# Optimization experiments

Hardware: AMD Instinct MI355X
Metric: run time of the kernel (lower is better)

Reference implementation:

```python
import jax, jax.numpy as jnp
import numpy as np

S = 4096   # decoder sequence length
T = 4096   # encoder sequence length
D = 2048   # x_size == qk_size (required for q @ k^T to typecheck)


def setup_inputs() -> dict:
    key = jax.random.key(0)
    k1, k2, k3, k4 = jax.random.split(key, 4)
    x_vectors = jax.random.normal(k1, (S, D), dtype=jnp.float32)
    enc_output = jax.random.normal(k2, (2, T, S), dtype=jnp.float32) * 0.02
    Wq = jax.random.normal(k3, (D, D), dtype=jnp.float32) * 0.02
    bq = jax.random.normal(k4, (D,), dtype=jnp.float32) * 0.02
    return {"x_vectors": x_vectors, "enc_output": enc_output, "Wq": Wq, "bq": bq}


def reference(x_vectors, enc_output, Wq, bq):
    # q = Linear(x): [S, D]
    q = x_vectors @ Wq.T + bq
    # k, v produced by matmul of encoder-output matrices with x: [T, D]
    k = enc_output[0] @ x_vectors
    v = enc_output[1] @ x_vectors
    # attention scores [S, T], scaled by sqrt(qk_size)
    e = (q @ k.T) / jnp.sqrt(jnp.float32(D))
    # softmax over dim=1 (last axis of the rank-2 score matrix)
    a = jax.nn.softmax(e, axis=1)
    # z = a @ v^T: [S, D]
    z = a @ v
    return z
```

## Files before the change

kernel.cpp:

```cpp
#include <hip/hip_runtime.h>


typedef __attribute__((ext_vector_type(8))) __bf16 bf16x8;
typedef __attribute__((ext_vector_type(4))) float f32x4;
typedef __attribute__((ext_vector_type(4))) unsigned short ushort4v;
typedef __attribute__((ext_vector_type(8))) unsigned short ushort8v;

#define S_DIM 4096
#define T_DIM 4096
#define D_DIM 2048

__device__ __forceinline__ unsigned short f2bf(float f) {
    unsigned int u = __float_as_uint(f);
    u += 0x7fffu + ((u >> 16) & 1u);
    return (unsigned short)(u >> 16);
}

__device__ __forceinline__ void block_sync() {
    __builtin_amdgcn_sched_barrier(0);
    __builtin_amdgcn_s_barrier();
    __builtin_amdgcn_sched_barrier(0);
}

#define GL(gptr, sptr)                                                        \
    __builtin_amdgcn_global_load_lds(                                         \
        (__attribute__((address_space(1))) void*)(void*)(gptr),               \
        (__attribute__((address_space(3))) void*)(sptr), 16, 0, 0)

__device__ __forceinline__ f32x4 MFMA(bf16x8 a, bf16x8 b, f32x4 c) {
    return __builtin_amdgcn_mfma_f32_16x16x32_bf16(a, b, c, 0, 0, 0);
}

__global__ __launch_bounds__(256)
void k_convert(const float* __restrict__ in, unsigned short* __restrict__ out, long n) {
    long i = ((long)blockIdx.x * blockDim.x + threadIdx.x) * 8;
    const long stride = (long)gridDim.x * blockDim.x * 8;
    for (; i < n; i += stride) {
        float4 a = *(const float4*)(in + i);
        float4 b = *(const float4*)(in + i + 4);
        ushort8v o;
        o[0] = f2bf(a.x); o[1] = f2bf(a.y); o[2] = f2bf(a.z); o[3] = f2bf(a.w);
        o[4] = f2bf(b.x); o[5] = f2bf(b.y); o[6] = f2bf(b.z); o[7] = f2bf(b.w);
        *(ushort8v*)(out + i) = o;
    }
}

__global__ __launch_bounds__(256)
void k_transpose(const float* __restrict__ in, unsigned short* __restrict__ out,
                 int R, int C) {
    __shared__ float tile[32][33];
    const int bx = blockIdx.x * 32;
    const int by = blockIdx.y * 32;
    const int tx = threadIdx.x;
    const int ty = threadIdx.y;
    #pragma unroll
    for (int i = 0; i < 32; i += 8)
        tile[ty + i][tx] = in[(long)(by + ty + i) * C + bx + tx];
    __syncthreads();
    #pragma unroll
    for (int i = 0; i < 32; i += 8)
        out[(long)(bx + ty + i) * R + by + tx] = f2bf(tile[tx][ty + i]);
}

__global__ __launch_bounds__(256)
void k_transpose_bf(const unsigned short* __restrict__ in,
                    unsigned short* __restrict__ out, int R, int C) {
    __shared__ unsigned short tile[32][33];
    const int bx = blockIdx.x * 32;
    const int by = blockIdx.y * 32;
    const int tx = threadIdx.x;
    const int ty = threadIdx.y;
    #pragma unroll
    for (int i = 0; i < 32; i += 8)
        tile[ty + i][tx] = in[(long)(by + ty + i) * C + bx + tx];
    __syncthreads();
    #pragma unroll
    for (int i = 0; i < 32; i += 8)
        out[(long)(bx + ty + i) * R + by + tx] = tile[tx][ty + i];
}

template<bool STG, bool PF, int VMW>
__device__ __forceinline__ void seg8(
    const unsigned short* (&gA)[2], const int (&ldA)[2],
    const unsigned short* (&gB)[2], const int (&ldB)[2],
    const char* cur, const char* nxt, char* stg, int arB, int brB,
    bf16x8 (&Ac)[8], bf16x8 (&B01c)[2], bf16x8 (&B23)[2],
    bf16x8 (&An)[8], bf16x8 (&B01n)[2],
    f32x4 (&acc)[8][4])
{
    B23[0] = *(const bf16x8*)(cur + brB + 2048);
    B23[1] = *(const bf16x8*)(cur + brB + 3072);
    if constexpr (STG) {
        GL(gA[0], stg + ldA[0]); gA[0] += 32;
        GL(gA[1], stg + ldA[1]); gA[1] += 32;
    }
    block_sync();
    asm volatile("s_waitcnt lgkmcnt(2)" ::: "memory");
    __builtin_amdgcn_sched_barrier(0);
    __builtin_amdgcn_s_setprio(1);
    #pragma unroll
    for (int m = 0; m < 8; ++m) {
        acc[m][0] = MFMA(Ac[m], B01c[0], acc[m][0]);
        acc[m][1] = MFMA(Ac[m], B01c[1], acc[m][1]);
    }
    __builtin_amdgcn_s_setprio(0);
    if constexpr (PF) {
        #pragma unroll
        for (int m = 0; m < 8; ++m)
            An[m] = *(const bf16x8*)(nxt + arB + m * 1024);
        B01n[0] = *(const bf16x8*)(nxt + brB);
        B01n[1] = *(const bf16x8*)(nxt + brB + 1024);
    }
    if constexpr (STG) {
        GL(gB[0], stg + ldB[0]); gB[0] += 32;
        GL(gB[1], stg + ldB[1]); gB[1] += 32;
    }
    if constexpr (VMW == 4)      asm volatile("s_waitcnt vmcnt(4)" ::: "memory");
    else if constexpr (VMW == 0) asm volatile("s_waitcnt vmcnt(0)" ::: "memory");
    block_sync();
    if constexpr (PF) asm volatile("s_waitcnt lgkmcnt(10)" ::: "memory");
    else              asm volatile("s_waitcnt lgkmcnt(0)" ::: "memory");
    __builtin_amdgcn_sched_barrier(0);
    __builtin_amdgcn_s_setprio(1);
    #pragma unroll
    for (int m = 0; m < 8; ++m) {
        acc[m][2] = MFMA(Ac[m], B23[0], acc[m][2]);
        acc[m][3] = MFMA(Ac[m], B23[1], acc[m][3]);
    }
    __builtin_amdgcn_s_setprio(0);
}

template<bool STG, bool PF, int VMW>
__device__ __forceinline__ void seg4(
    const unsigned short* (&gA)[2], const int (&ldA)[2],
    const unsigned short* (&gB)[2], const int (&ldB)[2],
    const char* nxt, char* stg, int arB, int brB,
    bf16x8 (&Ac)[4], bf16x8 (&Bc)[4],
    bf16x8 (&An)[4], bf16x8 (&Bn)[4],
    f32x4 (&acc)[4][4])
{
    if constexpr (PF) {
        #pragma unroll
        for (int m = 0; m < 4; ++m)
            An[m] = *(const bf16x8*)(nxt + arB + m * 1024);
        #pragma unroll
        for (int n = 0; n < 4; ++n)
            Bn[n] = *(const bf16x8*)(nxt + brB + n * 1024);
    }
    if constexpr (STG) {
        GL(gA[0], stg + ldA[0]); gA[0] += 32;
        GL(gB[0], stg + ldB[0]); gB[0] += 32;
        GL(gB[1], stg + ldB[1]); gB[1] += 32;
    }
    if constexpr (VMW == 3)      asm volatile("s_waitcnt vmcnt(3)" ::: "memory");
    else if constexpr (VMW == 0) asm volatile("s_waitcnt vmcnt(0)" ::: "memory");
    block_sync();
    if constexpr (PF) asm volatile("s_waitcnt lgkmcnt(8)" ::: "memory");
    else              asm volatile("s_waitcnt lgkmcnt(0)" ::: "memory");
    __builtin_amdgcn_sched_barrier(0);
    __builtin_amdgcn_s_setprio(1);
    #pragma unroll
    for (int m = 0; m < 4; ++m)
        #pragma unroll
        for (int n = 0; n < 4; ++n)
            acc[m][n] = MFMA(Ac[m], Bc[n], acc[m][n]);
    __builtin_amdgcn_s_setprio(0);
}

template<int MFR, int OUT_BF16, int HAS_BIAS>
__global__ __launch_bounds__(512, 2)
void k_gemm(const unsigned short* __restrict__ A,
            const unsigned short* __restrict__ B,
            const float* __restrict__ bias,
            void* __restrict__ C,
            int M, int N, int K, float alpha) {
    constexpr int BM   = MFR * 32;
    constexpr int LPTA = (BM * 4) / 512;
    constexpr int LDSA = BM * 64;
    constexpr int SLOT = LDSA + 16384;
    extern __shared__ __align__(16) char smem[];

    const int tid = threadIdx.x;
    const int l = tid & 63;
    const int w = tid >> 6;
    const int wr = w >> 2;
    const int wc = w & 3;

    const int gx = gridDim.x, gy = gridDim.y;
    const int flat = blockIdx.y * gx + blockIdx.x;
    const int per = (gx * gy) >> 3;
    const int wid = (flat & 7) * per + (flat >> 3);
    const int sc = wid / (gy * 4);
    const int rm = wid - sc * gy * 4;
    const int by = rm >> 2;
    const int bx = sc * 4 + (rm & 3);

    const long brow = (long)by * BM;
    const long bcol = (long)bx * 256;
    const int NT = K >> 5;

    const unsigned short* gA[2];
    int ldA[2];
    #pragma unroll
    for (int j = 0; j < LPTA; ++j) {
        const int q = (w * LPTA + j) * 64 + l;
        const int R = q >> 2;
        const int c = (q & 3) ^ ((R >> 1) & 3);
        gA[j] = A + (brow + R) * (long)K + c * 8;
        ldA[j] = q * 16;
    }
    const unsigned short* gB[2];
    int ldB[2];
    #pragma unroll
    for (int j = 0; j < 2; ++j) {
        const int q = (w * 2 + j) * 64 + l;
        const int R = q >> 2;
        const int c = (q & 3) ^ ((R >> 1) & 3);
        gB[j] = B + (bcol + R) * (long)K + c * 8;
        ldB[j] = LDSA + q * 16;
    }

    const int sAB = (((l >> 4) ^ ((l >> 1) & 3)) << 4);
    const int arB = (wr * (MFR * 16) + (l & 15)) * 64 + sAB;
    const int brB = LDSA + (wc * 64 + (l & 15)) * 64 + sAB;

    char* const b0 = smem;
    char* const b1 = smem + SLOT;
    char* const b2 = smem + 2 * SLOT;
    char* const b3 = smem + 3 * SLOT;

    f32x4 acc[MFR][4] = {};

    {
        char* d = smem;
        #pragma unroll
        for (int tt = 0; tt < 3; ++tt) {
            #pragma unroll
            for (int j = 0; j < LPTA; ++j) { GL(gA[j], d + ldA[j]); gA[j] += 32; }
            #pragma unroll
            for (int j = 0; j < 2; ++j)    { GL(gB[j], d + ldB[j]); gB[j] += 32; }
            d += SLOT;
        }
        if constexpr (MFR == 8) asm volatile("s_waitcnt vmcnt(4)" ::: "memory");
        else                    asm volatile("s_waitcnt vmcnt(3)" ::: "memory");
        block_sync();
    }

    if constexpr (MFR == 8) {
        bf16x8 Aa[8], Ab[8], Ba[2], Bb[2], B23[2];
        #pragma unroll
        for (int m = 0; m < 8; ++m) Aa[m] = *(const bf16x8*)(b0 + arB + m * 1024);
        Ba[0] = *(const bf16x8*)(b0 + brB);
        Ba[1] = *(const bf16x8*)(b0 + brB + 1024);

        for (int t = 0; t + 8 <= NT; t += 4) {
            seg8<true, true, 4>(gA, ldA, gB, ldB, b0, b1, b3, arB, brB,
                                Aa, Ba, B23, Ab, Bb, acc);
            seg8<true, true, 4>(gA, ldA, gB, ldB, b1, b2, b0, arB, brB,
                                Ab, Bb, B23, Aa, Ba, acc);
            seg8<true, true, 4>(gA, ldA, gB, ldB, b2, b3, b1, arB, brB,
                                Aa, Ba, B23, Ab, Bb, acc);
            seg8<true, true, 4>(gA, ldA, gB, ldB, b3, b0, b2, arB, brB,
                                Ab, Bb, B23, Aa, Ba, acc);
        }
        seg8<true,  true,  4>(gA, ldA, gB, ldB, b0, b1, b3, arB, brB,
                              Aa, Ba, B23, Ab, Bb, acc);
        seg8<false, true,  0>(gA, ldA, gB, ldB, b1, b2, b3, arB, brB,
                              Ab, Bb, B23, Aa, Ba, acc);
        seg8<false, true, -1>(gA, ldA, gB, ldB, b2, b3, b3, arB, brB,
                              Aa, Ba, B23, Ab, Bb, acc);
        seg8<false, false, -1>(gA, ldA, gB, ldB, b3, b0, b3, arB, brB,
                               Ab, Bb, B23, Aa, Ba, acc);
    } else {
        bf16x8 Aa[4], Ab[4], Ba[4], Bb[4];
        #pragma unroll
        for (int m = 0; m < 4; ++m) Aa[m] = *(const bf16x8*)(b0 + arB + m * 1024);
        #pragma unroll
        for (int n = 0; n < 4; ++n) Ba[n] = *(const bf16x8*)(b0 + brB + n * 1024);

        for (int t = 0; t + 8 <= NT; t += 4) {
            seg4<true, true, 3>(gA, ldA, gB, ldB, b1, b3, arB, brB, Aa, Ba, Ab, Bb, acc);
            seg4<true, true, 3>(gA, ldA, gB, ldB, b2, b0, arB, brB, Ab, Bb, Aa, Ba, acc);
            seg4<true, true, 3>(gA, ldA, gB, ldB, b3, b1, arB, brB, Aa, Ba, Ab, Bb, acc);
            seg4<true, true, 3>(gA, ldA, gB, ldB, b0, b2, arB, brB, Ab, Bb, Aa, Ba, acc);
        }
        seg4<true,  true,  3>(gA, ldA, gB, ldB, b1, b3, arB, brB, Aa, Ba, Ab, Bb, acc);
        seg4<false, true,  0>(gA, ldA, gB, ldB, b2, b3, arB, brB, Ab, Bb, Aa, Ba, acc);
        seg4<false, true, -1>(gA, ldA, gB, ldB, b3, b3, arB, brB, Aa, Ba, Ab, Bb, acc);
        seg4<false, false, -1>(gA, ldA, gB, ldB, b3, b3, arB, brB, Ab, Bb, Aa, Ba, acc);
    }

    const long crow0 = brow + wr * (MFR * 16) + (l >> 4) * 4;
    const long ccol0 = bcol + wc * 64 + (l & 15);
    #pragma unroll
    for (int n = 0; n < 4; ++n) {
        const long col = ccol0 + n * 16;
        const float bb = HAS_BIAS ? bias[col] : 0.0f;
        #pragma unroll
        for (int m = 0; m < MFR; ++m) {
            #pragma unroll
            for (int r = 0; r < 4; ++r) {
                const long row = crow0 + m * 16 + r;
                const float v = acc[m][n][r] * alpha + bb;
                if (OUT_BF16)
                    ((unsigned short*)C)[row * N + col] = f2bf(v);
                else
                    ((float*)C)[row * N + col] = v;
            }
        }
    }
}

__global__ __launch_bounds__(256)
void k_softmax(const float* __restrict__ E, unsigned short* __restrict__ A, int T) {
    const long row = blockIdx.x;
    const float* er = E + row * (long)T;
    const int t = threadIdx.x;
    const int l = t & 63;
    const int w = t >> 6;

    float4 v[4];
    float m = -3.4e38f;
    #pragma unroll
    for (int j = 0; j < 4; ++j) {
        v[j] = *(const float4*)(er + j * 1024 + t * 4);
        m = fmaxf(m, fmaxf(fmaxf(v[j].x, v[j].y), fmaxf(v[j].z, v[j].w)));
    }
    #pragma unroll
    for (int o = 32; o > 0; o >>= 1) m = fmaxf(m, __shfl_xor(m, o));

    __shared__ float redm[4];
    __shared__ float reds[4];
    if (l == 0) redm[w] = m;
    __syncthreads();
    m = fmaxf(fmaxf(redm[0], redm[1]), fmaxf(redm[2], redm[3]));

    float s = 0.f;
    #pragma unroll
    for (int j = 0; j < 4; ++j) {
        v[j].x = __expf(v[j].x - m); s += v[j].x;
        v[j].y = __expf(v[j].y - m); s += v[j].y;
        v[j].z = __expf(v[j].z - m); s += v[j].z;
        v[j].w = __expf(v[j].w - m); s += v[j].w;
    }
    #pragma unroll
    for (int o = 32; o > 0; o >>= 1) s += __shfl_xor(s, o);
    if (l == 0) reds[w] = s;
    __syncthreads();
    s = reds[0] + reds[1] + reds[2] + reds[3];
    const float inv = 1.0f / s;

    unsigned short* ar = A + row * (long)T;
    #pragma unroll
    for (int j = 0; j < 4; ++j) {
        ushort4v o4;
        o4[0] = f2bf(v[j].x * inv);
        o4[1] = f2bf(v[j].y * inv);
        o4[2] = f2bf(v[j].z * inv);
        o4[3] = f2bf(v[j].w * inv);
        *(ushort4v*)(ar + j * 1024 + t * 4) = o4;
    }
}

extern "C" void kernel_launch(void* const* d_in, const int* in_sizes, int n_in,
                              void* d_out, int out_size, void* d_ws, size_t ws_size,
                              hipStream_t stream) {
    const float* x   = (const float*)d_in[0];
    const float* enc = (const float*)d_in[1];
    const float* Wq  = (const float*)d_in[2];
    const float* bq  = (const float*)d_in[3];
    float* out = (float*)d_out;
    char* ws = (char*)d_ws;

    unsigned short* abf   = (unsigned short*)(ws);
    unsigned short* xT    = (unsigned short*)(ws);
    unsigned short* xbf   = (unsigned short*)(ws + (16L << 20));
    unsigned short* wqbf  = (unsigned short*)(ws + (32L << 20));
    unsigned short* qbf   = (unsigned short*)(ws + (40L << 20));
    unsigned short* kv    = (unsigned short*)(ws + (56L << 20));
    unsigned short* vT    = (unsigned short*)(ws + (88L << 20));
    unsigned short* encbf = (unsigned short*)(ws + (104L << 20));
    float*          e     = (float*)(ws + (104L << 20));

    k_convert<<<4096, 256, 0, stream>>>(x,   xbf,   (long)S_DIM * D_DIM);
    k_convert<<<4096, 256, 0, stream>>>(Wq,  wqbf,  (long)D_DIM * D_DIM);
    k_convert<<<4096, 256, 0, stream>>>(enc, encbf, 2L * T_DIM * S_DIM);
    k_transpose<<<dim3(D_DIM / 32, S_DIM / 32), dim3(32, 8), 0, stream>>>(x, xT, S_DIM, D_DIM);

    #define LAUNCH_G(MFRV, OB, HB, Ap, Bp, biasp, Cp, M_, N_, K_, al)                      \
        do {                                                                               \
            constexpr int smemB = (MFRV * 32 * 64 + 16384) * 4;                            \
            hipFuncSetAttribute((const void*)k_gemm<MFRV, OB, HB>,                         \
                                hipFuncAttributeMaxDynamicSharedMemorySize, smemB);        \
            k_gemm<MFRV, OB, HB><<<dim3((N_) / 256, (M_) / (MFRV * 32)), 512, smemB,       \
                                   stream>>>(Ap, Bp, biasp, Cp, M_, N_, K_, al);           \
        } while (0)

    LAUNCH_G(4, 1, 1, xbf, wqbf, bq, qbf, S_DIM, D_DIM, D_DIM, 1.0f);
    LAUNCH_G(8, 1, 0, encbf, xT, nullptr, kv, 2 * T_DIM, D_DIM, S_DIM, 1.0f);
    k_transpose_bf<<<dim3(D_DIM / 32, T_DIM / 32), dim3(32, 8), 0, stream>>>(
        kv + (long)T_DIM * D_DIM, vT, T_DIM, D_DIM);
    LAUNCH_G(8, 0, 0, qbf, kv, nullptr, e, S_DIM, T_DIM, D_DIM, 0.022097086912079608f);
    k_softmax<<<S_DIM, 256, 0, stream>>>(e, abf, T_DIM);
    LAUNCH_G(4, 0, 0, abf, vT, nullptr, out, S_DIM, D_DIM, T_DIM, 1.0f);
}
```

Before: 377.1 us.

## Store attention scores in bf16, fuse x convert into transpose, split MFR4 pipeline

The score GEMM now writes bf16 instead of fp32, and softmax reads bf16, which halves the traffic on the 4096x4096 score matrix. The x conversion is folded into the transpose kernel so x is read once, removing one launch. The MFR=4 GEMM path is restructured into two half-phases like the MFR=8 path, so B fragments load in halves with an extra barrier and more overlap. Rounding the scores to bf16 before softmax reduces accuracy of the logits.

```diff
diff --git a/kernel.cpp b/kernel.cpp
--- a/kernel.cpp
+++ b/kernel.cpp
@@ -27,7 +27,7 @@
         (__attribute__((address_space(1))) void*)(void*)(gptr),               \
         (__attribute__((address_space(3))) void*)(sptr), 16, 0, 0)
 
-__device__ __forceinline__ f32x4 MFMA(bf16x8 a, bf16x8 b, f32x4 c) {
+__device__ __forceinline__ f32x4 MFMA16(bf16x8 a, bf16x8 b, f32x4 c) {
     return __builtin_amdgcn_mfma_f32_16x16x32_bf16(a, b, c, 0, 0, 0);
 }
 
@@ -46,20 +46,24 @@
 }
 
 __global__ __launch_bounds__(256)
-void k_transpose(const float* __restrict__ in, unsigned short* __restrict__ out,
-                 int R, int C) {
+void k_transpose_dual(const float* __restrict__ in,
+                      unsigned short* __restrict__ outT,
+                      unsigned short* __restrict__ outN, int R, int C) {
     __shared__ float tile[32][33];
     const int bx = blockIdx.x * 32;
     const int by = blockIdx.y * 32;
     const int tx = threadIdx.x;
     const int ty = threadIdx.y;
     #pragma unroll
+    for (int i = 0; i < 32; i += 8) {
+        float v = in[(long)(by + ty + i) * C + bx + tx];
+        tile[ty + i][tx] = v;
+        outN[(long)(by + ty + i) * C + bx + tx] = f2bf(v);
+    }
+    __syncthreads();
+    #pragma unroll
     for (int i = 0; i < 32; i += 8)
-        tile[ty + i][tx] = in[(long)(by + ty + i) * C + bx + tx];
-    __syncthreads();
-    #pragma unroll
-    for (int i = 0; i < 32; i += 8)
-        out[(long)(bx + ty + i) * R + by + tx] = f2bf(tile[tx][ty + i]);
+        outT[(long)(bx + ty + i) * R + by + tx] = f2bf(tile[tx][ty + i]);
 }
 
 __global__ __launch_bounds__(256)
@@ -100,8 +104,8 @@
     __builtin_amdgcn_s_setprio(1);
     #pragma unroll
     for (int m = 0; m < 8; ++m) {
-        acc[m][0] = MFMA(Ac[m], B01c[0], acc[m][0]);
-        acc[m][1] = MFMA(Ac[m], B01c[1], acc[m][1]);
+        acc[m][0] = MFMA16(Ac[m], B01c[0], acc[m][0]);
+        acc[m][1] = MFMA16(Ac[m], B01c[1], acc[m][1]);
     }
     __builtin_amdgcn_s_setprio(0);
     if constexpr (PF) {
@@ -124,8 +128,8 @@
     __builtin_amdgcn_s_setprio(1);
     #pragma unroll
     for (int m = 0; m < 8; ++m) {
-        acc[m][2] = MFMA(Ac[m], B23[0], acc[m][2]);
-        acc[m][3] = MFMA(Ac[m], B23[1], acc[m][3]);
+        acc[m][2] = MFMA16(Ac[m], B23[0], acc[m][2]);
+        acc[m][3] = MFMA16(Ac[m], B23[1], acc[m][3]);
     }
     __builtin_amdgcn_s_setprio(0);
 }
@@ -134,36 +138,49 @@
 __device__ __forceinline__ void seg4(
     const unsigned short* (&gA)[2], const int (&ldA)[2],
     const unsigned short* (&gB)[2], const int (&ldB)[2],
-    const char* nxt, char* stg, int arB, int brB,
-    bf16x8 (&Ac)[4], bf16x8 (&Bc)[4],
-    bf16x8 (&An)[4], bf16x8 (&Bn)[4],
+    const char* cur, const char* nxt, char* stg, int arB, int brB,
+    bf16x8 (&Ac)[4], bf16x8 (&B01c)[2], bf16x8 (&B23)[2],
+    bf16x8 (&An)[4], bf16x8 (&B01n)[2],
     f32x4 (&acc)[4][4])
 {
+    B23[0] = *(const bf16x8*)(cur + brB + 2048);
+    B23[1] = *(const bf16x8*)(cur + brB + 3072);
+    if constexpr (STG) {
+        GL(gA[0], stg + ldA[0]); gA[0] += 32;
+    }
+    block_sync();
+    asm volatile("s_waitcnt lgkmcnt(2)" ::: "memory");
+    __builtin_amdgcn_sched_barrier(0);
+    __builtin_amdgcn_s_setprio(1);
+    #pragma unroll
+    for (int m = 0; m < 4; ++m) {
+        acc[m][0] = MFMA16(Ac[m], B01c[0], acc[m][0]);
+        acc[m][1] = MFMA16(Ac[m], B01c[1], acc[m][1]);
+    }
+    __builtin_amdgcn_s_setprio(0);
     if constexpr (PF) {
         #pragma unroll
         for (int m = 0; m < 4; ++m)
             An[m] = *(const bf16x8*)(nxt + arB + m * 1024);
-        #pragma unroll
-        for (int n = 0; n < 4; ++n)
-            Bn[n] = *(const bf16x8*)(nxt + brB + n * 1024);
+        B01n[0] = *(const bf16x8*)(nxt + brB);
+        B01n[1] = *(const bf16x8*)(nxt + brB + 1024);
     }
     if constexpr (STG) {
-        GL(gA[0], stg + ldA[0]); gA[0] += 32;
         GL(gB[0], stg + ldB[0]); gB[0] += 32;
         GL(gB[1], stg + ldB[1]); gB[1] += 32;
     }
     if constexpr (VMW == 3)      asm volatile("s_waitcnt vmcnt(3)" ::: "memory");
     else if constexpr (VMW == 0) asm volatile("s_waitcnt vmcnt(0)" ::: "memory");
     block_sync();
-    if constexpr (PF) asm volatile("s_waitcnt lgkmcnt(8)" ::: "memory");
+    if constexpr (PF) asm volatile("s_waitcnt lgkmcnt(6)" ::: "memory");
     else              asm volatile("s_waitcnt lgkmcnt(0)" ::: "memory");
     __builtin_amdgcn_sched_barrier(0);
     __builtin_amdgcn_s_setprio(1);
     #pragma unroll
-    for (int m = 0; m < 4; ++m)
-        #pragma unroll
-        for (int n = 0; n < 4; ++n)
-            acc[m][n] = MFMA(Ac[m], Bc[n], acc[m][n]);
+    for (int m = 0; m < 4; ++m) {
+        acc[m][2] = MFMA16(Ac[m], B23[0], acc[m][2]);
+        acc[m][3] = MFMA16(Ac[m], B23[1], acc[m][3]);
+    }
     __builtin_amdgcn_s_setprio(0);
 }
 
@@ -229,8 +246,6 @@
     char* const b2 = smem + 2 * SLOT;
     char* const b3 = smem + 3 * SLOT;
 
-    f32x4 acc[MFR][4] = {};
-
     {
         char* d = smem;
         #pragma unroll
@@ -253,6 +268,7 @@
         Ba[0] = *(const bf16x8*)(b0 + brB);
         Ba[1] = *(const bf16x8*)(b0 + brB + 1024);
 
+        f32x4 acc[8][4] = {};
         for (int t = 0; t + 8 <= NT; t += 4) {
             seg8<true, true, 4>(gA, ldA, gB, ldB, b0, b1, b3, arB, brB,
                                 Aa, Ba, B23, Ab, Bb, acc);
@@ -271,60 +287,94 @@
                               Aa, Ba, B23, Ab, Bb, acc);
         seg8<false, false, -1>(gA, ldA, gB, ldB, b3, b0, b3, arB, brB,
                                Ab, Bb, B23, Aa, Ba, acc);
+
+        const long crow0 = brow + wr * 128 + (l >> 4) * 4;
+        const long ccol0 = bcol + wc * 64 + (l & 15);
+        #pragma unroll
+        for (int n = 0; n < 4; ++n) {
+            const long col = ccol0 + n * 16;
+            const float bb = HAS_BIAS ? bias[col] : 0.0f;
+            #pragma unroll
+            for (int m = 0; m < 8; ++m) {
+                #pragma unroll
+                for (int r = 0; r < 4; ++r) {
+                    const long row = crow0 + m * 16 + r;
+                    const float v = acc[m][n][r] * alpha + bb;
+                    if (OUT_BF16)
+                        ((unsigned short*)C)[row * N + col] = f2bf(v);
+                    else
+                        ((float*)C)[row * N + col] = v;
+                }
+            }
+        }
     } else {
-        bf16x8 Aa[4], Ab[4], Ba[4], Bb[4];
+        bf16x8 Aa[4], Ab[4], Ba[2], Bb[2], B23[2];
         #pragma unroll
         for (int m = 0; m < 4; ++m) Aa[m] = *(const bf16x8*)(b0 + arB + m * 1024);
-        #pragma unroll
-        for (int n = 0; n < 4; ++n) Ba[n] = *(const bf16x8*)(b0 + brB + n * 1024);
-
+        Ba[0] = *(const bf16x8*)(b0 + brB);
+        Ba[1] = *(const bf16x8*)(b0 + brB + 1024);
+
+        f32x4 acc[4][4] = {};
         for (int t = 0; t + 8 <= NT; t += 4) {
-            seg4<true, true, 3>(gA, ldA, gB, ldB, b1, b3, arB, brB, Aa, Ba, Ab, Bb, acc);
-            seg4<true, true, 3>(gA, ldA, gB, ldB, b2, b0, arB, brB, Ab, Bb, Aa, Ba, acc);
-            seg4<true, true, 3>(gA, ldA, gB, ldB, b3, b1, arB, brB, Aa, Ba, Ab, Bb, acc);
-            seg4<true, true, 3>(gA, ldA, gB, ldB, b0, b2, arB, brB, Ab, Bb, Aa, Ba, acc);
-        }
-        seg4<true,  true,  3>(gA, ldA, gB, ldB, b1, b3, arB, brB, Aa, Ba, Ab, Bb, acc);
-        seg4<false, true,  0>(gA, ldA, gB, ldB, b2, b3, arB, brB, Ab, Bb, Aa, Ba, acc);
-        seg4<false, true, -1>(gA, ldA, gB, ldB, b3, b3, arB, brB, Aa, Ba, Ab, Bb, acc);
-        seg4<false, false, -1>(gA, ldA, gB, ldB, b3, b3, arB, brB, Ab, Bb, Aa, Ba, acc);
-    }
-
-    const long crow0 = brow + wr * (MFR * 16) + (l >> 4) * 4;
-    const long ccol0 = bcol + wc * 64 + (l & 15);
-    #pragma unroll
-    for (int n = 0; n < 4; ++n) {
-        const long col = ccol0 + n * 16;
-        const float bb = HAS_BIAS ? bias[col] : 0.0f;
-        #pragma unroll
-        for (int m = 0; m < MFR; ++m) {
+            seg4<true, true, 3>(gA, ldA, gB, ldB, b0, b1, b3, arB, brB,
+                                Aa, Ba, B23, Ab, Bb, acc);
+            seg4<true, true, 3>(gA, ldA, gB, ldB, b1, b2, b0, arB, brB,
+                                Ab, Bb, B23, Aa, Ba, acc);
+            seg4<true, true, 3>(gA, ldA, gB, ldB, b2, b3, b1, arB, brB,
+                                Aa, Ba, B23, Ab, Bb, acc);
+            seg4<true, true, 3>(gA, ldA, gB, ldB, b3, b0, b2, arB, brB,
+                                Ab, Bb, B23, Aa, Ba, acc);
+        }
+        seg4<true,  true,  3>(gA, ldA, gB, ldB, b0, b1, b3, arB, brB,
+                              Aa, Ba, B23, Ab, Bb, acc);
+        seg4<false, true,  0>(gA, ldA, gB, ldB, b1, b2, b3, arB, brB,
+                              Ab, Bb, B23, Aa, Ba, acc);
+        seg4<false, true, -1>(gA, ldA, gB, ldB, b2, b3, b3, arB, brB,
+                              Aa, Ba, B23, Ab, Bb, acc);
+        seg4<false, false, -1>(gA, ldA, gB, ldB, b3, b0, b3, arB, brB,
+                               Ab, Bb, B23, Aa, Ba, acc);
+
+        const long crow0 = brow + wr * 64 + (l >> 4) * 4;
+        const long ccol0 = bcol + wc * 64 + (l & 15);
+        #pragma unroll
+        for (int n = 0; n < 4; ++n) {
+            const long col = ccol0 + n * 16;
+            const float bb = HAS_BIAS ? bias[col] : 0.0f;
             #pragma unroll
-            for (int r = 0; r < 4; ++r) {
-                const long row = crow0 + m * 16 + r;
-                const float v = acc[m][n][r] * alpha + bb;
-                if (OUT_BF16)
-                    ((unsigned short*)C)[row * N + col] = f2bf(v);
-                else
-                    ((float*)C)[row * N + col] = v;
+            for (int m = 0; m < 4; ++m) {
+                #pragma unroll
+                for (int r = 0; r < 4; ++r) {
+                    const long row = crow0 + m * 16 + r;
+                    const float v = acc[m][n][r] * alpha + bb;
+                    if (OUT_BF16)
+                        ((unsigned short*)C)[row * N + col] = f2bf(v);
+                    else
+                        ((float*)C)[row * N + col] = v;
+                }
             }
         }
     }
 }
 
 __global__ __launch_bounds__(256)
-void k_softmax(const float* __restrict__ E, unsigned short* __restrict__ A, int T) {
+void k_softmax_bf(const unsigned short* __restrict__ E,
+                  unsigned short* __restrict__ A, int T) {
     const long row = blockIdx.x;
-    const float* er = E + row * (long)T;
+    const unsigned short* er = E + row * (long)T;
     const int t = threadIdx.x;
     const int l = t & 63;
     const int w = t >> 6;
 
-    float4 v[4];
+    float v[16];
     float m = -3.4e38f;
     #pragma unroll
-    for (int j = 0; j < 4; ++j) {
-        v[j] = *(const float4*)(er + j * 1024 + t * 4);
-        m = fmaxf(m, fmaxf(fmaxf(v[j].x, v[j].y), fmaxf(v[j].z, v[j].w)));
+    for (int j = 0; j < 2; ++j) {
+        ushort8v u = *(const ushort8v*)(er + j * 2048 + t * 8);
+        #pragma unroll
+        for (int i = 0; i < 8; ++i) {
+            v[j * 8 + i] = __uint_as_float((unsigned int)u[i] << 16);
+            m = fmaxf(m, v[j * 8 + i]);
+        }
     }
     #pragma unroll
     for (int o = 32; o > 0; o >>= 1) m = fmaxf(m, __shfl_xor(m, o));
@@ -337,11 +387,9 @@
 
     float s = 0.f;
     #pragma unroll
-    for (int j = 0; j < 4; ++j) {
-        v[j].x = __expf(v[j].x - m); s += v[j].x;
-        v[j].y = __expf(v[j].y - m); s += v[j].y;
-        v[j].z = __expf(v[j].z - m); s += v[j].z;
-        v[j].w = __expf(v[j].w - m); s += v[j].w;
+    for (int i = 0; i < 16; ++i) {
+        v[i] = __expf(v[i] - m);
+        s += v[i];
     }
     #pragma unroll
     for (int o = 32; o > 0; o >>= 1) s += __shfl_xor(s, o);
@@ -352,13 +400,11 @@
 
     unsigned short* ar = A + row * (long)T;
     #pragma unroll
-    for (int j = 0; j < 4; ++j) {
-        ushort4v o4;
-        o4[0] = f2bf(v[j].x * inv);
-        o4[1] = f2bf(v[j].y * inv);
-        o4[2] = f2bf(v[j].z * inv);
-        o4[3] = f2bf(v[j].w * inv);
-        *(ushort4v*)(ar + j * 1024 + t * 4) = o4;
+    for (int j = 0; j < 2; ++j) {
+        ushort8v o8;
+        #pragma unroll
+        for (int i = 0; i < 8; ++i) o8[i] = f2bf(v[j * 8 + i] * inv);
+        *(ushort8v*)(ar + j * 2048 + t * 8) = o8;
     }
 }
 
@@ -380,12 +426,12 @@
     unsigned short* kv    = (unsigned short*)(ws + (56L << 20));
     unsigned short* vT    = (unsigned short*)(ws + (88L << 20));
     unsigned short* encbf = (unsigned short*)(ws + (104L << 20));
-    float*          e     = (float*)(ws + (104L << 20));
-
-    k_convert<<<4096, 256, 0, stream>>>(x,   xbf,   (long)S_DIM * D_DIM);
+    unsigned short* ebf   = (unsigned short*)(ws + (104L << 20));
+
     k_convert<<<4096, 256, 0, stream>>>(Wq,  wqbf,  (long)D_DIM * D_DIM);
     k_convert<<<4096, 256, 0, stream>>>(enc, encbf, 2L * T_DIM * S_DIM);
-    k_transpose<<<dim3(D_DIM / 32, S_DIM / 32), dim3(32, 8), 0, stream>>>(x, xT, S_DIM, D_DIM);
+    k_transpose_dual<<<dim3(D_DIM / 32, S_DIM / 32), dim3(32, 8), 0, stream>>>(
+        x, xT, xbf, S_DIM, D_DIM);
 
     #define LAUNCH_G(MFRV, OB, HB, Ap, Bp, biasp, Cp, M_, N_, K_, al)                      \
         do {                                                                               \
@@ -400,7 +446,7 @@
     LAUNCH_G(8, 1, 0, encbf, xT, nullptr, kv, 2 * T_DIM, D_DIM, S_DIM, 1.0f);
     k_transpose_bf<<<dim3(D_DIM / 32, T_DIM / 32), dim3(32, 8), 0, stream>>>(
         kv + (long)T_DIM * D_DIM, vT, T_DIM, D_DIM);
-    LAUNCH_G(8, 0, 0, qbf, kv, nullptr, e, S_DIM, T_DIM, D_DIM, 0.022097086912079608f);
-    k_softmax<<<S_DIM, 256, 0, stream>>>(e, abf, T_DIM);
+    LAUNCH_G(8, 1, 0, qbf, kv, nullptr, ebf, S_DIM, T_DIM, D_DIM, 0.022097086912079608f);
+    k_softmax_bf<<<S_DIM, 256, 0, stream>>>(ebf, abf, T_DIM);
     LAUNCH_G(4, 0, 0, abf, vT, nullptr, out, S_DIM, D_DIM, T_DIM, 1.0f);
 }
```

New measurement: 360.9 us. 4.3% less time.
